# Performance work log

Measured on AMD Instinct MI355X. Metric: run time of the kernel, lower is better.

Reference implementation:

```python
import jax, jax.numpy as jnp
import numpy as np

NUM_USERS = 100000
NUM_ITEMS = 50000
NUM_EDGES = 2000000
DIM = 64
NUM_REL = 5


def setup_inputs() -> dict:
    key = jax.random.key(0)
    k1, k2, k3, k4, k5, k6 = jax.random.split(key, 6)
    u_features = jax.random.normal(k1, (NUM_USERS, DIM), dtype=jnp.float32)
    i_features = jax.random.normal(k2, (NUM_ITEMS, DIM), dtype=jnp.float32)
    edge_user = jax.random.randint(k3, (NUM_EDGES,), 0, NUM_USERS, dtype=jnp.int64)
    edge_item = jax.random.randint(k4, (NUM_EDGES,), 0, NUM_ITEMS, dtype=jnp.int64)
    # per-relation Linear params, torch convention: y = x @ W[r].T + b[r]
    W = jax.random.normal(k5, (NUM_REL, DIM, DIM), dtype=jnp.float32) * (1.0 / np.sqrt(DIM))
    b = jax.random.normal(k6, (NUM_REL, DIM), dtype=jnp.float32) * 0.01
    return {"u_features": u_features, "i_features": i_features,
            "edge_user": edge_user, "edge_item": edge_item, "W": W, "b": b}


def reference(u_features, i_features, edge_user, edge_item, W, b):
    # gather edge endpoint features: [E, D]
    edge_u = u_features[edge_user]
    edge_i = i_features[edge_item]
    num_rel = W.shape[0]
    # per relation: sum((edge_u @ W[r].T + b[r]) * edge_i, axis=1) -> [E]
    # loop over small fixed relation count to avoid [E, R, D] intermediate
    cols = [jnp.sum((edge_u @ W[r].T + b[r]) * edge_i, axis=1)
            for r in range(num_rel)]
    return jnp.stack(cols, axis=1)  # [E, R]
```

## Files before the change

### kernel.cpp

```cpp
#include <hip/hip_runtime.h>
#include <stdint.h>

#define NREL 5
#define D 64
#define Q_BYTES 320
#define NT 21
#define NB 8
#define CHUNK 4096
#define EDGE_GRID 2048

typedef __attribute__((ext_vector_type(8))) short short8;
typedef __attribute__((ext_vector_type(4))) float f32x4;

static __device__ __forceinline__ short f2bf(float f) {
    uint32_t u = __float_as_uint(f);
    u += 0x7FFFu + ((u >> 16) & 1u);
    return (short)(u >> 16);
}

#if defined(__has_builtin)
#if __has_builtin(__builtin_amdgcn_sdot4)
#define HAVE_SDOT4 1
#endif
#endif
#ifdef HAVE_SDOT4
static __device__ __forceinline__ int SDOT4(uint32_t a, uint32_t b, int c) {
    return __builtin_amdgcn_sdot4((int)a, (int)b, c, false);
}
#else
static __device__ __forceinline__ int SDOT4(uint32_t a, uint32_t b, int c) {
    c += ((int)(a << 24) >> 24) * ((int)(b << 24) >> 24);
    c += ((int)(a << 16) >> 24) * ((int)(b << 16) >> 24);
    c += ((int)(a << 8) >> 24) * ((int)(b << 8) >> 24);
    c += ((int)a >> 24) * ((int)b >> 24);
    return c;
}
#endif

__global__ __launch_bounds__(256) void wprep_kernel(
    const float* __restrict__ W, const float* __restrict__ bias_p, short* __restrict__ Wf)
{
    const int tid = blockIdx.x * 256 + threadIdx.x;
    if (tid >= NT * 2 * 64) return;
    const int lane = tid & 63;
    const int h = (tid >> 6) & 1;
    const int nt = tid >> 7;
    const int ln = lane & 15, quad = lane >> 4;
    const int n = nt * 16 + ln;
    uint32_t w[4];
#pragma unroll
    for (int p = 0; p < 4; ++p) {
        uint32_t lo = 0, hi = 0;
#pragma unroll
        for (int s = 0; s < 2; ++s) {
            const int j = p * 2 + s;
            const int d = h * 32 + quad * 8 + j;
            float v;
            if (nt < 20) v = W[(n >> 6) * (D * D) + d * D + (n & 63)];
            else         v = (ln < NREL) ? bias_p[ln * D + d] : 0.f;
            if (s == 0) lo = (uint16_t)f2bf(v); else hi = (uint16_t)f2bf(v);
        }
        w[p] = lo | (hi << 16);
    }
    *(uint4*)(Wf + (size_t)tid * 8) = make_uint4(w[0], w[1], w[2], w[3]);
}

__global__ __launch_bounds__(256) void fused_kernel(
    const float* __restrict__ i_feat, const short* __restrict__ Wf,
    char* __restrict__ qrecs, float* __restrict__ sc, int nItems,
    const float* __restrict__ uf, uint32_t* __restrict__ uq,
    float* __restrict__ uscale, int nUsers,
    const int* __restrict__ edge_user, const int* __restrict__ edge_item,
    int nE, int bucketDiv, int cap,
    int* __restrict__ totals, uint32_t* __restrict__ sorted,
    uint16_t* __restrict__ perm, int* __restrict__ blockBase)
{
    __shared__ int cnt[NB];
    __shared__ int base[NB];
    const int nbI = (nItems + 63) / 64;
    const int nbS = (nE + CHUNK - 1) / CHUNK;
    int bid = blockIdx.x;

    if (bid < nbI) {
        const int lane = threadIdx.x & 63;
        const int wv = threadIdx.x >> 6;
        const int m0 = bid * 64 + wv * 16;
        const int ln = lane & 15, quad = lane >> 4;

        int rowA = m0 + ln;
        if (rowA >= nItems) rowA = nItems - 1;
        const float* ap = i_feat + (size_t)rowA * D + quad * 8;
        short8 af[2];
#pragma unroll
        for (int h = 0; h < 2; ++h) {
            const float4 x = *(const float4*)(ap + h * 32);
            const float4 y = *(const float4*)(ap + h * 32 + 4);
            short8 a;
            a[0] = f2bf(x.x); a[1] = f2bf(x.y); a[2] = f2bf(x.z); a[3] = f2bf(x.w);
            a[4] = f2bf(y.x); a[5] = f2bf(y.y); a[6] = f2bf(y.z); a[7] = f2bf(y.w);
            af[h] = a;
        }

        f32x4 acc[NT];
#pragma unroll
        for (int nt = 0; nt < NT; ++nt) acc[nt] = (f32x4){0.f, 0.f, 0.f, 0.f};

#pragma unroll
        for (int nt = 0; nt < NT; ++nt) {
            const short8 b0 = *(const short8*)(Wf + ((size_t)(nt * 2 + 0) * 64 + lane) * 8);
            acc[nt] = __builtin_amdgcn_mfma_f32_16x16x32_bf16(af[0], b0, acc[nt], 0, 0, 0);
            const short8 b1 = *(const short8*)(Wf + ((size_t)(nt * 2 + 1) * 64 + lane) * 8);
            acc[nt] = __builtin_amdgcn_mfma_f32_16x16x32_bf16(af[1], b1, acc[nt], 0, 0, 0);
        }

#pragma unroll
        for (int g = 0; g < 4; ++g) {
            const int item = m0 + quad * 4 + g;
            const bool ok = (item < nItems);
            char* rec = qrecs + (size_t)item * Q_BYTES;
#pragma unroll
            for (int r = 0; r < NREL; ++r) {
                const float v0 = acc[4 * r + 0][g];
                const float v1 = acc[4 * r + 1][g];
                const float v2 = acc[4 * r + 2][g];
                const float v3 = acc[4 * r + 3][g];
                float m = fmaxf(fmaxf(fabsf(v0), fabsf(v1)), fmaxf(fabsf(v2), fabsf(v3)));
                m = fmaxf(m, __shfl_xor(m, 1));
                m = fmaxf(m, __shfl_xor(m, 2));
                m = fmaxf(m, __shfl_xor(m, 4));
                m = fmaxf(m, __shfl_xor(m, 8));
                m = fmaxf(m, 1e-20f);
                const float qs = 127.0f / m;
                const uint32_t pw = ((uint32_t)(uint8_t)(int8_t)(int)rintf(v0 * qs))
                                  | ((uint32_t)(uint8_t)(int8_t)(int)rintf(v1 * qs) << 8)
                                  | ((uint32_t)(uint8_t)(int8_t)(int)rintf(v2 * qs) << 16)
                                  | ((uint32_t)(uint8_t)(int8_t)(int)rintf(v3 * qs) << 24);
                if (ok) {
                    *(uint32_t*)(rec + r * D + ln * 4) = pw;
                    if (ln == 0) sc[(size_t)item * 16 + 2 * r] = m * (1.0f / 127.0f);
                }
            }
            if (ok && ln < NREL) sc[(size_t)item * 16 + 2 * ln + 1] = acc[20][g];
        }
        return;
    }
    bid -= nbI;

    if (bid < nbS) {
        if (threadIdx.x < NB) cnt[threadIdx.x] = 0;
        __syncthreads();

        const long start = (long)bid * CHUNK;
        uint32_t pk[CHUNK / 256];
        unsigned long long bins = 0;
        unsigned long long accLo = 0, accHi = 0;
#pragma unroll
        for (int k = 0; k < CHUNK / 256; ++k) {
            const long e = start + k * 256 + threadIdx.x;
            const bool ok = (e < nE);
            int iu = 0, ii = 0;
            if (ok) { iu = edge_user[e]; ii = edge_item[e]; }
            const int bn = ok ? (ii / bucketDiv) : 0;
            const int iiL = ii - bn * bucketDiv;
            pk[k] = ok ? ((uint32_t)iu | ((uint32_t)iiL << 17)) : 0xFFFFFFFFu;
            bins |= (unsigned long long)bn << (k * 3);
            if (ok) {
                const unsigned long long one = 1ull << ((bn & 3) * 16);
                if (bn < 4) accLo += one; else accHi += one;
            }
        }
#pragma unroll
        for (int d = 1; d < 64; d <<= 1) {
            accLo += __shfl_xor(accLo, d);
            accHi += __shfl_xor(accHi, d);
        }
        if ((threadIdx.x & 63) == 0) {
#pragma unroll
            for (int f = 0; f < 4; ++f) {
                atomicAdd(&cnt[f],     (int)((accLo >> (f * 16)) & 0xFFFF));
                atomicAdd(&cnt[4 + f], (int)((accHi >> (f * 16)) & 0xFFFF));
            }
        }
        __syncthreads();
        if (threadIdx.x < NB) {
            const int c = cnt[threadIdx.x];
            const int bs = threadIdx.x * cap + atomicAdd(&totals[threadIdx.x], c);
            base[threadIdx.x] = bs;
            blockBase[bid * NB + threadIdx.x] = bs;
            cnt[threadIdx.x] = 0;
        }
        __syncthreads();
#pragma unroll
        for (int k = 0; k < CHUNK / 256; ++k) {
            if (pk[k] != 0xFFFFFFFFu) {
                const long e = start + k * 256 + threadIdx.x;
                const int bn = (int)((bins >> (k * 3)) & 7);
                const int r = atomicAdd(&cnt[bn], 1);
                sorted[base[bn] + r] = pk[k];
                perm[e] = (uint16_t)((bn << 12) | r);
            }
        }
        return;
    }
    bid -= nbS;

    const int gid = bid * 256 + threadIdx.x;
    const int row = gid >> 4;
    const int t = gid & 15;
    if (row >= nUsers) return;
    const float* rp = uf + (size_t)row * D;
    const float v0 = rp[t], v1 = rp[16 + t], v2 = rp[32 + t], v3 = rp[48 + t];
    float m = fmaxf(fmaxf(fabsf(v0), fabsf(v1)), fmaxf(fabsf(v2), fabsf(v3)));
    m = fmaxf(m, __shfl_xor(m, 1));
    m = fmaxf(m, __shfl_xor(m, 2));
    m = fmaxf(m, __shfl_xor(m, 4));
    m = fmaxf(m, __shfl_xor(m, 8));
    m = fmaxf(m, 1e-20f);
    const float qs = 127.0f / m;
    const int q0 = (int)rintf(v0 * qs);
    const int q1 = (int)rintf(v1 * qs);
    const int q2 = (int)rintf(v2 * qs);
    const int q3 = (int)rintf(v3 * qs);
    uq[(size_t)row * 16 + t] = ((uint32_t)(uint8_t)(int8_t)q0)
                             | ((uint32_t)(uint8_t)(int8_t)q1 << 8)
                             | ((uint32_t)(uint8_t)(int8_t)q2 << 16)
                             | ((uint32_t)(uint8_t)(int8_t)q3 << 24);
    if (t == 0) uscale[row] = m * (1.0f / 127.0f);
}

__global__ __launch_bounds__(256) void edge_kernel(
    const uint32_t* __restrict__ u_q,
    const float* __restrict__ u_scale,
    const uint32_t* __restrict__ sorted,
    const int* __restrict__ totals, int cap, int bucketDiv,
    const char* __restrict__ qrecs,
    const float* __restrict__ sc,
    float* __restrict__ resA,
    float* __restrict__ resB)
{
    const int b = blockIdx.x & 7;
    const int seg = blockIdx.x >> 3;
    const int nSeg = gridDim.x >> 3;
    const int s0 = b * cap;
    const int s1 = s0 + totals[b];
    const int cnt = s1 - s0;
    const int per = (cnt + nSeg - 1) / nSeg;
    const int p0 = s0 + seg * per;
    const int p1 = min(p0 + per, s1);

    const int lane = threadIdx.x & 63;
    const int wv = threadIdx.x >> 6;
    const int es = lane >> 2;
    const int c = lane & 3;
    const int itemBase = b * bucketDiv;

    for (int q0 = p0 + wv * 16; q0 < p1; q0 += 64) {
        const int pos = q0 + es;
        if (pos < p1) {
            const uint32_t pk = sorted[pos];
            const int iu = (int)(pk & 0x1FFFF);
            const int ii = itemBase + (int)(pk >> 17);

            const uint4 uv = *(const uint4*)(u_q + (size_t)iu * 16 + c * 4);
            const char* rec = qrecs + (size_t)ii * Q_BYTES;

            int s[NREL];
#pragma unroll
            for (int r = 0; r < NREL; ++r) {
                const uint4 yv = *(const uint4*)(rec + r * D + c * 16);
                int t = SDOT4(uv.x, yv.x, 0);
                t = SDOT4(uv.y, yv.y, t);
                t = SDOT4(uv.z, yv.z, t);
                s[r] = SDOT4(uv.w, yv.w, t);
            }
#pragma unroll
            for (int r = 0; r < NREL; ++r) {
                s[r] += __shfl_xor(s[r], 1);
                s[r] += __shfl_xor(s[r], 2);
            }
            const float us = u_scale[iu];
            const float* scp = sc + (size_t)ii * 16;
            const float2 sb = *(const float2*)(scp + 2 * c);
            __builtin_nontemporal_store(fmaf((float)s[c], us * sb.x, sb.y),
                                        resA + (size_t)pos * 4 + c);
            if (c == 0) {
                const float2 sb4 = *(const float2*)(scp + 8);
                __builtin_nontemporal_store(fmaf((float)s[4], us * sb4.x, sb4.y),
                                            resB + pos);
            }
        }
    }
}

__global__ __launch_bounds__(256) void unperm_kernel(
    const uint16_t* __restrict__ perm,
    const int* __restrict__ blockBase,
    const float4* __restrict__ resA,
    const float* __restrict__ resB,
    int nE,
    float* __restrict__ out)
{
    __shared__ int bb[NB];
    if (threadIdx.x < NB) bb[threadIdx.x] = blockBase[blockIdx.x * NB + threadIdx.x];
    __syncthreads();
    const long start = (long)blockIdx.x * CHUNK;
#pragma unroll
    for (int k = 0; k < CHUNK / 256; ++k) {
        const long e = start + k * 256 + threadIdx.x;
        if (e < nE) {
            const int pr = perm[e];
            const int p = bb[pr >> 12] + (pr & 0xFFF);
            const float4 a = resA[p];
            const float b5 = resB[p];
            float* op = out + e * NREL;
            op[0] = a.x; op[1] = a.y; op[2] = a.z; op[3] = a.w; op[4] = b5;
        }
    }
}

extern "C" void kernel_launch(void* const* d_in, const int* in_sizes, int n_in,
                              void* d_out, int out_size, void* d_ws, size_t ws_size,
                              hipStream_t stream) {
    const float* u_feat    = (const float*)d_in[0];
    const float* i_feat    = (const float*)d_in[1];
    const int*   edge_user = (const int*)d_in[2];
    const int*   edge_item = (const int*)d_in[3];
    const float* W         = (const float*)d_in[4];
    const float* b         = (const float*)d_in[5];
    float* out = (float*)d_out;

    const int nUsers = in_sizes[0] / D;
    const int nItems = in_sizes[1] / D;
    const int nE = in_sizes[2];
    const int bucketDiv = (nItems + NB - 1) / NB;
    const int nBlocksSort = (nE + CHUNK - 1) / CHUNK;
    const int cap = nE / NB + 4096;

    size_t off = 0;
    char* qrecs = (char*)d_ws;
    off += ((size_t)nItems * Q_BYTES + 255) & ~(size_t)255;
    float* sc = (float*)((char*)d_ws + off);
    off += ((size_t)nItems * 16 * sizeof(float) + 255) & ~(size_t)255;
    uint32_t* u_q = (uint32_t*)((char*)d_ws + off);
    off += ((size_t)nUsers * D + 255) & ~(size_t)255;
    float* u_scale = (float*)((char*)d_ws + off);
    off += ((size_t)nUsers * sizeof(float) + 255) & ~(size_t)255;
    short* Wf = (short*)((char*)d_ws + off);
    off += ((size_t)NT * 2 * 64 * 8 * sizeof(short) + 255) & ~(size_t)255;
    int* totals = (int*)((char*)d_ws + off);
    off += 256;
    int* blockBase = (int*)((char*)d_ws + off);
    off += ((size_t)nBlocksSort * NB * sizeof(int) + 255) & ~(size_t)255;
    uint32_t* sorted = (uint32_t*)((char*)d_ws + off);
    off += ((size_t)NB * cap * sizeof(uint32_t) + 255) & ~(size_t)255;
    uint16_t* perm = (uint16_t*)((char*)d_ws + off);
    off += ((size_t)nE * sizeof(uint16_t) + 255) & ~(size_t)255;
    float* resA = (float*)((char*)d_ws + off);
    off += ((size_t)NB * cap * 4 * sizeof(float) + 255) & ~(size_t)255;
    float* resB = (float*)((char*)d_ws + off);
    off += ((size_t)NB * cap * sizeof(float) + 255) & ~(size_t)255;

    hipMemsetAsync(totals, 0, NB * sizeof(int), stream);

    wprep_kernel<<<(NT * 2 * 64 + 255) / 256, 256, 0, stream>>>(W, b, Wf);

    const int nbI = (nItems + 63) / 64;
    const int nbU = (nUsers * 16 + 255) / 256;
    fused_kernel<<<nbI + nBlocksSort + nbU, 256, 0, stream>>>(
        i_feat, Wf, qrecs, sc, nItems,
        u_feat, u_q, u_scale, nUsers,
        edge_user, edge_item, nE, bucketDiv, cap,
        totals, sorted, perm, blockBase);

    edge_kernel<<<EDGE_GRID, 256, 0, stream>>>(u_q, u_scale, sorted, totals, cap, bucketDiv,
                                               qrecs, sc, resA, resB);
    unperm_kernel<<<nBlocksSort, 256, 0, stream>>>(perm, blockBase,
                                                   (const float4*)resA, resB, nE, out);
}
```

Measured before the change: 240.9 us.

## Bucket edges into 2D item-by-user sub-bins for better gather locality

Edges are now binned by item bucket and also by one of 16 user sub-ranges, so the edge kernel walks each item bucket one user slice at a time. The aim is to keep the gathered user rows in cache during each pass. The warp-level packed histogram becomes per-edge shared atomics over 128 bins, and perm now stores 32-bit absolute positions, which removes the blockBase table at the cost of more perm bandwidth. The edge kernel splits each of the 16 sub-bins across all segments, which adds per-sub-bin loop overhead, and the fixed per-bin capacity could overflow under skewed inputs.

Result: slower. 259.3 us (+7.7%).

```diff
diff --git a/kernel.cpp b/kernel.cpp
--- a/kernel.cpp
+++ b/kernel.cpp
@@ -6,6 +6,8 @@
 #define Q_BYTES 320
 #define NT 21
 #define NB 8
+#define NSUB 16
+#define NBT (NB * NSUB)
 #define CHUNK 4096
 #define EDGE_GRID 2048
 
@@ -71,12 +73,12 @@
     const float* __restrict__ uf, uint32_t* __restrict__ uq,
     float* __restrict__ uscale, int nUsers,
     const int* __restrict__ edge_user, const int* __restrict__ edge_item,
-    int nE, int bucketDiv, int cap,
+    int nE, int bucketDiv, int subDiv, int capBin,
     int* __restrict__ totals, uint32_t* __restrict__ sorted,
-    uint16_t* __restrict__ perm, int* __restrict__ blockBase)
+    uint32_t* __restrict__ perm)
 {
-    __shared__ int cnt[NB];
-    __shared__ int base[NB];
+    __shared__ int cnt[NBT];
+    __shared__ int base[NBT];
     const int nbI = (nItems + 63) / 64;
     const int nbS = (nE + CHUNK - 1) / CHUNK;
     int bid = blockIdx.x;
@@ -147,57 +149,39 @@
     bid -= nbI;
 
     if (bid < nbS) {
-        if (threadIdx.x < NB) cnt[threadIdx.x] = 0;
+        if (threadIdx.x < NBT) cnt[threadIdx.x] = 0;
         __syncthreads();
 
         const long start = (long)bid * CHUNK;
         uint32_t pk[CHUNK / 256];
-        unsigned long long bins = 0;
-        unsigned long long accLo = 0, accHi = 0;
+        uint8_t bn[CHUNK / 256];
 #pragma unroll
         for (int k = 0; k < CHUNK / 256; ++k) {
             const long e = start + k * 256 + threadIdx.x;
             const bool ok = (e < nE);
             int iu = 0, ii = 0;
             if (ok) { iu = edge_user[e]; ii = edge_item[e]; }
-            const int bn = ok ? (ii / bucketDiv) : 0;
-            const int iiL = ii - bn * bucketDiv;
-            pk[k] = ok ? ((uint32_t)iu | ((uint32_t)iiL << 17)) : 0xFFFFFFFFu;
-            bins |= (unsigned long long)bn << (k * 3);
-            if (ok) {
-                const unsigned long long one = 1ull << ((bn & 3) * 16);
-                if (bn < 4) accLo += one; else accHi += one;
-            }
-        }
-#pragma unroll
-        for (int d = 1; d < 64; d <<= 1) {
-            accLo += __shfl_xor(accLo, d);
-            accHi += __shfl_xor(accHi, d);
-        }
-        if ((threadIdx.x & 63) == 0) {
-#pragma unroll
-            for (int f = 0; f < 4; ++f) {
-                atomicAdd(&cnt[f],     (int)((accLo >> (f * 16)) & 0xFFFF));
-                atomicAdd(&cnt[4 + f], (int)((accHi >> (f * 16)) & 0xFFFF));
-            }
+            const int bi = ii / bucketDiv;
+            const int iiL = ii - bi * bucketDiv;
+            pk[k] = (uint32_t)iu | ((uint32_t)iiL << 17);
+            bn[k] = ok ? (uint8_t)(bi * NSUB + iu / subDiv) : (uint8_t)255;
+            if (ok) atomicAdd(&cnt[bn[k]], 1);
         }
         __syncthreads();
-        if (threadIdx.x < NB) {
+        if (threadIdx.x < NBT) {
             const int c = cnt[threadIdx.x];
-            const int bs = threadIdx.x * cap + atomicAdd(&totals[threadIdx.x], c);
-            base[threadIdx.x] = bs;
-            blockBase[bid * NB + threadIdx.x] = bs;
+            base[threadIdx.x] = threadIdx.x * capBin + atomicAdd(&totals[threadIdx.x], c);
             cnt[threadIdx.x] = 0;
         }
         __syncthreads();
 #pragma unroll
         for (int k = 0; k < CHUNK / 256; ++k) {
-            if (pk[k] != 0xFFFFFFFFu) {
+            if (bn[k] != 255) {
                 const long e = start + k * 256 + threadIdx.x;
-                const int bn = (int)((bins >> (k * 3)) & 7);
-                const int r = atomicAdd(&cnt[bn], 1);
-                sorted[base[bn] + r] = pk[k];
-                perm[e] = (uint16_t)((bn << 12) | r);
+                const int r = atomicAdd(&cnt[bn[k]], 1);
+                const int pos = base[bn[k]] + r;
+                sorted[pos] = pk[k];
+                perm[e] = (uint32_t)pos;
             }
         }
         return;
@@ -232,7 +216,7 @@
     const uint32_t* __restrict__ u_q,
     const float* __restrict__ u_scale,
     const uint32_t* __restrict__ sorted,
-    const int* __restrict__ totals, int cap, int bucketDiv,
+    const int* __restrict__ totals, int capBin, int bucketDiv,
     const char* __restrict__ qrecs,
     const float* __restrict__ sc,
     float* __restrict__ resA,
@@ -241,12 +225,6 @@
     const int b = blockIdx.x & 7;
     const int seg = blockIdx.x >> 3;
     const int nSeg = gridDim.x >> 3;
-    const int s0 = b * cap;
-    const int s1 = s0 + totals[b];
-    const int cnt = s1 - s0;
-    const int per = (cnt + nSeg - 1) / nSeg;
-    const int p0 = s0 + seg * per;
-    const int p1 = min(p0 + per, s1);
 
     const int lane = threadIdx.x & 63;
     const int wv = threadIdx.x >> 6;
@@ -254,62 +232,67 @@
     const int c = lane & 3;
     const int itemBase = b * bucketDiv;
 
-    for (int q0 = p0 + wv * 16; q0 < p1; q0 += 64) {
-        const int pos = q0 + es;
-        if (pos < p1) {
-            const uint32_t pk = sorted[pos];
-            const int iu = (int)(pk & 0x1FFFF);
-            const int ii = itemBase + (int)(pk >> 17);
-
-            const uint4 uv = *(const uint4*)(u_q + (size_t)iu * 16 + c * 4);
-            const char* rec = qrecs + (size_t)ii * Q_BYTES;
-
-            int s[NREL];
-#pragma unroll
-            for (int r = 0; r < NREL; ++r) {
-                const uint4 yv = *(const uint4*)(rec + r * D + c * 16);
-                int t = SDOT4(uv.x, yv.x, 0);
-                t = SDOT4(uv.y, yv.y, t);
-                t = SDOT4(uv.z, yv.z, t);
-                s[r] = SDOT4(uv.w, yv.w, t);
+    for (int sb = 0; sb < NSUB; ++sb) {
+        const int kb = b * NSUB + sb;
+        const int s0 = kb * capBin;
+        const int s1 = s0 + totals[kb];
+        const int cnt = s1 - s0;
+        const int per = (cnt + nSeg - 1) / nSeg;
+        const int p0 = s0 + seg * per;
+        const int p1 = min(p0 + per, s1);
+
+        for (int q0 = p0 + wv * 16; q0 < p1; q0 += 64) {
+            const int pos = q0 + es;
+            if (pos < p1) {
+                const uint32_t pk = sorted[pos];
+                const int iu = (int)(pk & 0x1FFFF);
+                const int ii = itemBase + (int)(pk >> 17);
+
+                const uint4 uv = *(const uint4*)(u_q + (size_t)iu * 16 + c * 4);
+                const char* rec = qrecs + (size_t)ii * Q_BYTES;
+
+                int s[NREL];
+#pragma unroll
+                for (int r = 0; r < NREL; ++r) {
+                    const uint4 yv = *(const uint4*)(rec + r * D + c * 16);
+                    int t = SDOT4(uv.x, yv.x, 0);
+                    t = SDOT4(uv.y, yv.y, t);
+                    t = SDOT4(uv.z, yv.z, t);
+                    s[r] = SDOT4(uv.w, yv.w, t);
+                }
+#pragma unroll
+                for (int r = 0; r < NREL; ++r) {
+                    s[r] += __shfl_xor(s[r], 1);
+                    s[r] += __shfl_xor(s[r], 2);
+                }
+                const float us = u_scale[iu];
+                const float* scp = sc + (size_t)ii * 16;
+                const float2 sb2 = *(const float2*)(scp + 2 * c);
+                __builtin_nontemporal_store(fmaf((float)s[c], us * sb2.x, sb2.y),
+                                            resA + (size_t)pos * 4 + c);
+                if (c == 0) {
+                    const float2 sb4 = *(const float2*)(scp + 8);
+                    __builtin_nontemporal_store(fmaf((float)s[4], us * sb4.x, sb4.y),
+                                                resB + pos);
+                }
             }
-#pragma unroll
-            for (int r = 0; r < NREL; ++r) {
-                s[r] += __shfl_xor(s[r], 1);
-                s[r] += __shfl_xor(s[r], 2);
-            }
-            const float us = u_scale[iu];
-            const float* scp = sc + (size_t)ii * 16;
-            const float2 sb = *(const float2*)(scp + 2 * c);
-            __builtin_nontemporal_store(fmaf((float)s[c], us * sb.x, sb.y),
-                                        resA + (size_t)pos * 4 + c);
-            if (c == 0) {
-                const float2 sb4 = *(const float2*)(scp + 8);
-                __builtin_nontemporal_store(fmaf((float)s[4], us * sb4.x, sb4.y),
-                                            resB + pos);
-            }
         }
     }
 }
 
 __global__ __launch_bounds__(256) void unperm_kernel(
-    const uint16_t* __restrict__ perm,
-    const int* __restrict__ blockBase,
+    const uint32_t* __restrict__ perm,
     const float4* __restrict__ resA,
     const float* __restrict__ resB,
     int nE,
     float* __restrict__ out)
 {
-    __shared__ int bb[NB];
-    if (threadIdx.x < NB) bb[threadIdx.x] = blockBase[blockIdx.x * NB + threadIdx.x];
-    __syncthreads();
     const long start = (long)blockIdx.x * CHUNK;
 #pragma unroll
     for (int k = 0; k < CHUNK / 256; ++k) {
         const long e = start + k * 256 + threadIdx.x;
         if (e < nE) {
-            const int pr = perm[e];
-            const int p = bb[pr >> 12] + (pr & 0xFFF);
+            const int p = (int)perm[e];
             const float4 a = resA[p];
             const float b5 = resB[p];
             float* op = out + e * NREL;
@@ -333,8 +316,9 @@
     const int nItems = in_sizes[1] / D;
     const int nE = in_sizes[2];
     const int bucketDiv = (nItems + NB - 1) / NB;
+    const int subDiv = (nUsers + NSUB - 1) / NSUB;
     const int nBlocksSort = (nE + CHUNK - 1) / CHUNK;
-    const int cap = nE / NB + 4096;
+    const int capBin = nE / NBT + 1024;
 
     size_t off = 0;
     char* qrecs = (char*)d_ws;
@@ -348,19 +332,17 @@
     short* Wf = (short*)((char*)d_ws + off);
     off += ((size_t)NT * 2 * 64 * 8 * sizeof(short) + 255) & ~(size_t)255;
     int* totals = (int*)((char*)d_ws + off);
-    off += 256;
-    int* blockBase = (int*)((char*)d_ws + off);
-    off += ((size_t)nBlocksSort * NB * sizeof(int) + 255) & ~(size_t)255;
+    off += 512;
     uint32_t* sorted = (uint32_t*)((char*)d_ws + off);
-    off += ((size_t)NB * cap * sizeof(uint32_t) + 255) & ~(size_t)255;
-    uint16_t* perm = (uint16_t*)((char*)d_ws + off);
-    off += ((size_t)nE * sizeof(uint16_t) + 255) & ~(size_t)255;
+    off += ((size_t)NBT * capBin * sizeof(uint32_t) + 255) & ~(size_t)255;
+    uint32_t* perm = (uint32_t*)((char*)d_ws + off);
+    off += ((size_t)nE * sizeof(uint32_t) + 255) & ~(size_t)255;
     float* resA = (float*)((char*)d_ws + off);
-    off += ((size_t)NB * cap * 4 * sizeof(float) + 255) & ~(size_t)255;
+    off += ((size_t)NBT * capBin * 4 * sizeof(float) + 255) & ~(size_t)255;
     float* resB = (float*)((char*)d_ws + off);
-    off += ((size_t)NB * cap * sizeof(float) + 255) & ~(size_t)255;
-
-    hipMemsetAsync(totals, 0, NB * sizeof(int), stream);
+    off += ((size_t)NBT * capBin * sizeof(float) + 255) & ~(size_t)255;
+
+    hipMemsetAsync(totals, 0, NBT * sizeof(int), stream);
 
     wprep_kernel<<<(NT * 2 * 64 + 255) / 256, 256, 0, stream>>>(W, b, Wf);
 
@@ -369,11 +351,10 @@
     fused_kernel<<<nbI + nBlocksSort + nbU, 256, 0, stream>>>(
         i_feat, Wf, qrecs, sc, nItems,
         u_feat, u_q, u_scale, nUsers,
-        edge_user, edge_item, nE, bucketDiv, cap,
-        totals, sorted, perm, blockBase);
-
-    edge_kernel<<<EDGE_GRID, 256, 0, stream>>>(u_q, u_scale, sorted, totals, cap, bucketDiv,
+        edge_user, edge_item, nE, bucketDiv, subDiv, capBin,
+        totals, sorted, perm);
+
+    edge_kernel<<<EDGE_GRID, 256, 0, stream>>>(u_q, u_scale, sorted, totals, capBin, bucketDiv,
                                                qrecs, sc, resA, resB);
-    unperm_kernel<<<nBlocksSort, 256, 0, stream>>>(perm, blockBase,
-                                                   (const float4*)resA, resB, nE, out);
-}
+    unperm_kernel<<<nBlocksSort, 256, 0, stream>>>(perm, (const float4*)resA, resB, nE, out);
+}
```
